# Optimization experiments

Hardware: AMD Instinct MI355X
Metric: run time of the kernel (lower is better)

## Reference

```python
import jax, jax.numpy as jnp
import numpy as np

B, NQ, NKV = 2, 1024, 4096
DQ = 1024          # query_dim == context_dim
H, DH = 16, 64     # heads, dim_head
INNER = H * DH     # 1024
SCALE = DH ** -0.5


def setup_inputs() -> dict:
    key = jax.random.key(0)
    ks = jax.random.split(key, 6)
    s = 1.0 / np.sqrt(DQ)
    return {
        "x": jax.random.normal(ks[0], (B, NQ, DQ), dtype=jnp.float32),
        "context": jax.random.normal(ks[1], (B, NKV, DQ), dtype=jnp.float32),
        "Wq": jax.random.normal(ks[2], (DQ, INNER), dtype=jnp.float32) * s,
        "Wkv": jax.random.normal(ks[3], (DQ, 2 * INNER), dtype=jnp.float32) * s,
        "Wout": jax.random.normal(ks[4], (INNER, DQ), dtype=jnp.float32) * (1.0 / np.sqrt(INNER)),
        "b_out": jax.random.normal(ks[5], (DQ,), dtype=jnp.float32) * 0.01,
    }


def _split_heads(t):
    # b n (h d) -> b h n d
    b, n, _ = t.shape
    return t.reshape(b, n, H, DH).transpose(0, 2, 1, 3)


def reference(x, context, Wq, Wkv, Wout, b_out):
    q = x @ Wq                       # [B, NQ, INNER]
    kv = context @ Wkv               # [B, NKV, 2*INNER]
    k, v = jnp.split(kv, 2, axis=-1)
    q, k, v = map(_split_heads, (q, k, v))          # [B, H, n, DH]
    sim = jnp.einsum("bhid,bhjd->bhij", q, k) * SCALE  # [B, H, NQ, NKV]
    attn = jax.nn.softmax(sim, axis=-1)
    out = jnp.einsum("bhij,bhjd->bhid", attn, v)       # [B, H, NQ, DH]
    out = out.transpose(0, 2, 1, 3).reshape(B, NQ, INNER)  # (b h) n d -> b n (h d)
    return out @ Wout + b_out
```

## Files before the change

kernel.cpp:

```cpp
#include <hip/hip_runtime.h>
#include <stdint.h>

#define B_    2
#define NQ_   1024
#define NKV_  4096
#define DQ_   1024
#define H_    16
#define DH_   64
#define INNER_ 1024

typedef unsigned short u16;
typedef uint32_t u32;
typedef __bf16 bf16x8 __attribute__((ext_vector_type(8)));
typedef float  f32x4  __attribute__((ext_vector_type(4)));

__device__ __forceinline__ u16 f2bf(float x) {
  union { float f; uint32_t u; } v; v.f = x;
  uint32_t r = v.u + 0x7FFFu + ((v.u >> 16) & 1u);
  return (u16)(r >> 16);
}
__device__ __forceinline__ u32 pack2(float a, float b) {
  return (u32)f2bf(a) | ((u32)f2bf(b) << 16);
}
__device__ __forceinline__ u32 pack2rn(float a, float b) {
  union { float f; u32 u; } x, y; x.f = a; y.f = b;
  return __builtin_amdgcn_perm(y.u + 0x8000u, x.u + 0x8000u, 0x07060302u);
}
__device__ __forceinline__ float bf2f(u16 s) {
  union { float f; uint32_t u; } v; v.u = ((uint32_t)s) << 16; return v.f;
}

__device__ __forceinline__ void gload16(const void* g, void* l) {
  __builtin_amdgcn_global_load_lds((const __attribute__((address_space(1))) void*)g,
                                   (__attribute__((address_space(3))) void*)l,
                                   16, 0, 0);
}

__global__ __launch_bounds__(256) void prep(const float* __restrict__ x,
                                            const float* __restrict__ ctx,
                                            const float* __restrict__ Wq,
                                            const float* __restrict__ Wkv,
                                            const float* __restrict__ Wout,
                                            u16* __restrict__ xb,
                                            u16* __restrict__ ctxb,
                                            u16* __restrict__ WqT,
                                            u16* __restrict__ WkvT,
                                            u16* __restrict__ WoutT) {
  int bid = blockIdx.x;
  if (bid < 640) {
    const float* src; u16* dst; int fbase;
    if (bid < 128) { src = x;   dst = xb;   fbase = bid * 4096; }
    else           { src = ctx; dst = ctxb; fbase = (bid - 128) * 4096; }
#pragma unroll
    for (int u = 0; u < 16; ++u) {
      int i = (fbase + u * 256 + threadIdx.x) * 4;
      float4 v = *(const float4*)(src + i);
      uint2 o; o.x = pack2(v.x, v.y); o.y = pack2(v.z, v.w);
      *(uint2*)(dst + i) = o;
    }
    return;
  }
  __shared__ float tile[64][65];
  const float* W; u16* Wt; int K, N, local, ntm;
  int b2 = bid - 640;
  if (b2 < 256)      { W = Wq;   Wt = WqT;   K = 1024; N = 1024; local = b2;       ntm = 15; }
  else if (b2 < 768) { W = Wkv;  Wt = WkvT;  K = 1024; N = 2048; local = b2 - 256; ntm = 31; }
  else               { W = Wout; Wt = WoutT; K = 1024; N = 1024; local = b2 - 768; ntm = 15; }
  int n0 = (local & ntm) * 64;
  int k0 = (local > ntm ? local >> (ntm == 15 ? 4 : 5) : 0) * 64;
  k0 = (ntm == 15) ? (local >> 4) * 64 : (local >> 5) * 64;
  int tx = threadIdx.x & 63, ty = threadIdx.x >> 6;
  for (int i = ty; i < 64; i += 4)
    tile[i][tx] = W[(size_t)(k0 + i) * N + n0 + tx];
  __syncthreads();
  int tx2 = threadIdx.x & 31, ty2 = threadIdx.x >> 5;
  for (int j = ty2; j < 64; j += 8)
    *(u32*)&Wt[(size_t)(n0 + j) * K + k0 + tx2 * 2] =
        pack2(tile[tx2 * 2][j], tile[tx2 * 2 + 1][j]);
}

__global__ __launch_bounds__(512, 2) void kv_gemm(const u16* __restrict__ ctxb,
                                                  const u16* __restrict__ WkvT,
                                                  u16* __restrict__ kb,
                                                  u16* __restrict__ vTb) {
  __shared__ __align__(16) u16 As[2][256 * 64];
  __shared__ __align__(16) u16 Bs[2][256 * 64];
  const int tid = threadIdx.x;
  const int lane = tid & 63;
  const int w = tid >> 6;
  const int wr = w >> 2, wc = w & 3;
  const int l15 = lane & 15, quad = lane >> 4;
  const int K = 1024;

  int bid = blockIdx.x;
  int wgid = (bid & 7) * 32 + (bid >> 3);
  const int tm = wgid >> 3, tn = wgid & 7;
  const int m0 = tm * 256, n0 = tn * 256;
  const u16* Ag = ctxb + (size_t)m0 * K;
  const u16* Bg = WkvT + (size_t)n0 * K;

  size_t offA[2][2], offB[2][2];
#pragma unroll
  for (int ah = 0; ah < 2; ++ah)
#pragma unroll
    for (int p = 0; p < 2; ++p) {
      int c = p * 512 + (w << 6) + lane;
      int s = ah * 128 + (c >> 3);
      int col = ((c & 7) ^ (s & 7)) << 3;
      int rA = ((s >> 6) & 1) * 128 + ((s >> 7) & 1) * 64 + (s & 63);
      int rB = ((s >> 5) & 3) * 64 + ((s >> 7) & 1) * 32 + (s & 31);
      offA[ah][p] = (size_t)rA * 1024 + col;
      offB[ah][p] = (size_t)rB * 1024 + col;
    }

#define STAGE_A(bufi, ah, kk) do { \
    gload16(Ag + offA[ah][0] + (kk), &As[bufi][(ah) * 8192 + (w << 9)]); \
    gload16(Ag + offA[ah][1] + (kk), &As[bufi][(ah) * 8192 + 4096 + (w << 9)]); \
  } while (0)
#define STAGE_B(bufi, bh, kk) do { \
    gload16(Bg + offB[bh][0] + (kk), &Bs[bufi][(bh) * 8192 + (w << 9)]); \
    gload16(Bg + offB[bh][1] + (kk), &Bs[bufi][(bh) * 8192 + 4096 + (w << 9)]); \
  } while (0)
#define LDA2(dst, i8, bufi) do { \
    const int _s = ((i8) >> 2) * 128 + wr * 64 + ((i8) & 3) * 16 + l15; \
    const u16* _p = &As[bufi][_s * 64]; const int _x = _s & 7; \
    dst[0] = *(const bf16x8*)&_p[(quad ^ _x) << 3]; \
    dst[1] = *(const bf16x8*)&_p[((quad + 4) ^ _x) << 3]; \
  } while (0)
#define LDB2(dst, j, bufi) do { \
    const int _s = ((j) >> 1) * 128 + wc * 32 + ((j) & 1) * 16 + l15; \
    const u16* _p = &Bs[bufi][_s * 64]; const int _x = _s & 7; \
    dst[0] = *(const bf16x8*)&_p[(quad ^ _x) << 3]; \
    dst[1] = *(const bf16x8*)&_p[((quad + 4) ^ _x) << 3]; \
  } while (0)
#define MF(i0, j0, bb) do { \
    _Pragma("unroll") \
    for (int _i = 0; _i < 4; ++_i) { \
      acc[(i0) + _i][(j0)    ] = __builtin_amdgcn_mfma_f32_16x16x32_bf16(a[_i][0], bb[0][0], acc[(i0) + _i][(j0)    ], 0, 0, 0); \
      acc[(i0) + _i][(j0)    ] = __builtin_amdgcn_mfma_f32_16x16x32_bf16(a[_i][1], bb[0][1], acc[(i0) + _i][(j0)    ], 0, 0, 0); \
      acc[(i0) + _i][(j0) + 1] = __builtin_amdgcn_mfma_f32_16x16x32_bf16(a[_i][0], bb[1][0], acc[(i0) + _i][(j0) + 1], 0, 0, 0); \
      acc[(i0) + _i][(j0) + 1] = __builtin_amdgcn_mfma_f32_16x16x32_bf16(a[_i][1], bb[1][1], acc[(i0) + _i][(j0) + 1], 0, 0, 0); \
    } \
  } while (0)
#define BAR()   __builtin_amdgcn_s_barrier()
#define LGKM0() asm volatile("s_waitcnt lgkmcnt(0)" ::: "memory")

  f32x4 acc[8][4] = {};
  bf16x8 a[4][2], b[2][2], c2[2][2];

  STAGE_A(0, 0, 0);
  STAGE_B(0, 0, 0);
  STAGE_B(0, 1, 0);
  STAGE_A(0, 1, 0);
  STAGE_A(1, 0, 64);
  STAGE_B(1, 0, 64);
  STAGE_B(1, 1, 64);
  asm volatile("s_waitcnt vmcnt(6)" ::: "memory");
  BAR();

#define HALF(bufi, kAb, kNext, STG, WMID, WEND) do { \
    LDB2(b[0], 0, bufi); LDB2(b[1], 1, bufi); \
    LDA2(a[0], 0, bufi); LDA2(a[1], 1, bufi); LDA2(a[2], 2, bufi); LDA2(a[3], 3, bufi); \
    if (kAb >= 0) STAGE_A((bufi) ^ 1, 1, kAb); \
    BAR(); LGKM0(); \
    __builtin_amdgcn_s_setprio(1); MF(0, 0, b); __builtin_amdgcn_s_setprio(0); \
    BAR(); \
    LDB2(c2[0], 2, bufi); LDB2(c2[1], 3, bufi); \
    if (STG) STAGE_A(bufi, 0, kNext); \
    BAR(); LGKM0(); \
    __builtin_amdgcn_s_setprio(1); MF(0, 2, c2); __builtin_amdgcn_s_setprio(0); \
    BAR(); \
    LDA2(a[0], 4, bufi); LDA2(a[1], 5, bufi); LDA2(a[2], 6, bufi); LDA2(a[3], 7, bufi); \
    if (STG) STAGE_B(bufi, 0, kNext); \
    BAR(); LGKM0(); \
    __builtin_amdgcn_s_setprio(1); MF(4, 0, b); __builtin_amdgcn_s_setprio(0); \
    BAR(); \
    if (STG) STAGE_B(bufi, 1, kNext); \
    BAR(); \
    __builtin_amdgcn_s_setprio(1); MF(4, 2, c2); __builtin_amdgcn_s_setprio(0); \
    WMID; \
    BAR(); \
  } while (0)

  for (int i = 0; i < 7; ++i) {
    const int k2 = i * 128;
    HALF(0, k2 + 64, k2 + 128, 1,
         asm volatile("s_waitcnt vmcnt(6)" ::: "memory"), );
    HALF(1, k2 + 128, k2 + 192, 1,
         asm volatile("s_waitcnt vmcnt(6)" ::: "memory"), );
  }
  HALF(0, 960, 0, 0,
       asm volatile("s_waitcnt vmcnt(0)" ::: "memory"), );
  HALF(1, -1, 0, 0, , );

#undef HALF
#undef BAR
#undef LGKM0

  if (tn < 4) {
#pragma unroll
    for (int i8 = 0; i8 < 8; ++i8)
#pragma unroll
      for (int j = 0; j < 4; ++j) {
        int col = n0 + wc * 64 + j * 16 + l15;
#pragma unroll
        for (int r = 0; r < 4; ++r) {
          int row = m0 + wr * 128 + i8 * 16 + quad * 4 + r;
          kb[(size_t)row * 1024 + col] = f2bf(acc[i8][j][r]);
        }
      }
  } else {
    const int bb_ = m0 >> 12;
#pragma unroll
    for (int i8 = 0; i8 < 8; ++i8) {
      int kvr = (m0 & 4095) + wr * 128 + i8 * 16 + quad * 4;
#pragma unroll
      for (int j = 0; j < 4; ++j) {
        int c = (n0 - 1024) + wc * 64 + j * 16 + l15;
        int h = c >> 6, dh = c & 63;
        uint2 st;
        st.x = pack2(acc[i8][j][0], acc[i8][j][1]);
        st.y = pack2(acc[i8][j][2], acc[i8][j][3]);
        *(uint2*)&vTb[((size_t)((bb_ * 16 + h) * 64 + dh)) * NKV_ + kvr] = st;
      }
    }
  }
#undef STAGE_A
#undef STAGE_B
#undef LDA2
#undef LDB2
#undef MF
}

__global__ __launch_bounds__(256) void out_gemm(const u16* __restrict__ A,
                                                const u16* __restrict__ Bt,
                                                float* __restrict__ Cout,
                                                const float* __restrict__ bias) {
  __shared__ __align__(16) u16 As[3][64 * 32];
  __shared__ __align__(16) u16 Bs[3][128 * 32];
  const int tid = threadIdx.x;
  const int lane = tid & 63;
  const int w = tid >> 6;
  const int wr = w >> 1, wc = w & 1;
  const int l15 = lane & 15, quad = lane >> 4;
  const int unit = blockIdx.x;
  const int m0 = (unit >> 3) * 64, n0 = (unit & 7) * 128;
  const int K = 1024, N = 1024;

  const u16* Ab = A + (size_t)m0 * K;
  const u16* Bb = Bt + (size_t)n0 * K;
  f32x4 acc[2][4] = {};

  const int ar = tid >> 2, ac = (tid & 3) << 3;
  const int q1 = w * 64 + lane, q2 = q1 + 256;
  const int br1 = q1 >> 2, bc1 = (q1 & 3) << 3;
  const int br2 = q2 >> 2, bc2 = (q2 & 3) << 3;

#define STG(bi, k0) do { \
    gload16(Ab + (size_t)ar * K + (k0) + ac, &As[bi][w * 512]); \
    gload16(Bb + (size_t)br1 * K + (k0) + bc1, &Bs[bi][w * 512]); \
    gload16(Bb + (size_t)br2 * K + (k0) + bc2, &Bs[bi][2048 + w * 512]); \
  } while (0)

  STG(0, 0);
  STG(1, 32);
  asm volatile("s_waitcnt vmcnt(3)" ::: "memory");
  __builtin_amdgcn_s_barrier();

  for (int it = 0; it < 32; ++it) {
    const int cur = it % 3;
    bf16x8 af[2], bfr[4];
#pragma unroll
    for (int i = 0; i < 2; ++i)
      af[i] = *(const bf16x8*)&As[cur][(wr * 32 + i * 16 + l15) * 32 + quad * 8];
#pragma unroll
    for (int j = 0; j < 4; ++j)
      bfr[j] = *(const bf16x8*)&Bs[cur][(wc * 64 + j * 16 + l15) * 32 + quad * 8];
    if (it + 2 < 32) STG((it + 2) % 3, (it + 2) * 32);
    __builtin_amdgcn_s_barrier();
    asm volatile("s_waitcnt lgkmcnt(0)" ::: "memory");
    __builtin_amdgcn_s_setprio(1);
#pragma unroll
    for (int i = 0; i < 2; ++i)
#pragma unroll
      for (int j = 0; j < 4; ++j)
        acc[i][j] = __builtin_amdgcn_mfma_f32_16x16x32_bf16(af[i], bfr[j], acc[i][j], 0, 0, 0);
    __builtin_amdgcn_s_setprio(0);
    if (it + 2 < 32)      { asm volatile("s_waitcnt vmcnt(3)" ::: "memory"); }
    else if (it + 2 == 32){ asm volatile("s_waitcnt vmcnt(0)" ::: "memory"); }
    __builtin_amdgcn_s_barrier();
  }
#undef STG

#pragma unroll
  for (int i = 0; i < 2; ++i)
#pragma unroll
    for (int j = 0; j < 4; ++j) {
      int col = n0 + wc * 64 + j * 16 + l15;
      float bv = bias[col];
#pragma unroll
      for (int r = 0; r < 4; ++r) {
        int row = m0 + wr * 32 + i * 16 + quad * 4 + r;
        Cout[(size_t)row * N + col] = acc[i][j][r] + bv;
      }
    }
}

__global__ __launch_bounds__(256, 2) void attn_kernel(const u16* __restrict__ xb,
                                                      const u16* __restrict__ WqT,
                                                      const u16* __restrict__ kb,
                                                      const u16* __restrict__ vT,
                                                      u16* __restrict__ attn_out) {
  __shared__ __align__(16) u16 Ks[128 * 64];
  __shared__ __align__(16) u16 Vs[64 * 128];
  __shared__ __align__(16) u32 P32[4 * 4 * 16 * 20];
  __shared__ float Lr[4][4][16];

  const int tid = threadIdx.x;
  const int lane = tid & 63;
  const int w = tid >> 6;
  const int l15 = lane & 15, quad = lane >> 4;
  const int bh = blockIdx.x, b = bh >> 4, h = bh & 15;
  const int q0 = blockIdx.y * 64;

  const float SC = 0.125f * 1.44269504088896340736f;
  union { u16 s[8]; bf16x8 v; } qf[4][2];

  {
    const u16* Axb = xb + (size_t)(b * NQ_ + q0) * 1024;
    const u16* Bwq = WqT + (size_t)(h * 64) * 1024;
    const int c1 = tid, c2 = tid + 256;
    const int r1 = c1 >> 3, g1 = c1 & 7;
    const int r2 = c2 >> 3, g2 = c2 & 7;
    const size_t sO1 = (size_t)r1 * 1024 + (size_t)((g1 ^ (r1 & 7)) << 3);
    const size_t sO2 = (size_t)r2 * 1024 + (size_t)((g2 ^ (r2 & 7)) << 3);
    f32x4 qacc[4] = {};
    const int x7 = l15 & 7;
    for (int k0 = 0; k0 < 1024; k0 += 64) {
      __syncthreads();
      gload16(Axb + sO1 + k0, &Ks[w * 512]);
      gload16(Axb + sO2 + k0, &Ks[2048 + w * 512]);
      gload16(Bwq + sO1 + k0, &Ks[4096 + w * 512]);
      gload16(Bwq + sO2 + k0, &Ks[6144 + w * 512]);
      __syncthreads();
      bf16x8 af[2], bfr[4][2];
#pragma unroll
      for (int kc = 0; kc < 2; ++kc) {
        af[kc] = *(const bf16x8*)&Ks[(w * 16 + l15) * 64 + (((kc * 4 + quad) ^ x7) << 3)];
#pragma unroll
        for (int j = 0; j < 4; ++j)
          bfr[j][kc] = *(const bf16x8*)
            &Ks[4096 + (j * 16 + l15) * 64 + (((kc * 4 + quad) ^ x7) << 3)];
      }
#pragma unroll
      for (int j = 0; j < 4; ++j) {
        qacc[j] = __builtin_amdgcn_mfma_f32_16x16x32_bf16(af[0], bfr[j][0], qacc[j], 0, 0, 0);
        qacc[j] = __builtin_amdgcn_mfma_f32_16x16x32_bf16(af[1], bfr[j][1], qacc[j], 0, 0, 0);
      }
    }
    float* Q64 = (float*)Vs;
#pragma unroll
    for (int j = 0; j < 4; ++j)
#pragma unroll
      for (int r = 0; r < 4; ++r) {
        int row = w * 16 + quad * 4 + r;
        Q64[row * 64 + ((j * 16 + l15) ^ ((row & 7) * 8))] = qacc[j][r];
      }
    __syncthreads();
#pragma unroll
    for (int t = 0; t < 4; ++t)
#pragma unroll
      for (int kc = 0; kc < 2; ++kc) {
        const float* qp = Q64 + (t * 16 + l15) * 64 + (((kc * 4 + quad) ^ x7) * 8);
        f32x4 lo = *(const f32x4*)qp;
        f32x4 hi = *(const f32x4*)(qp + 4);
#pragma unroll
        for (int e = 0; e < 4; ++e) {
          qf[t][kc].s[e]     = f2bf(lo[e] * SC);
          qf[t][kc].s[e + 4] = f2bf(hi[e] * SC);
        }
      }
    __syncthreads();
  }

#define STAGEKV(j0) do { \
    _Pragma("unroll") \
    for (int i_ = 0; i_ < 4; ++i_) { \
      int s_ = i_ * 256 + tid; \
      int kr = s_ >> 3, kg = (s_ ^ kr) & 7; \
      gload16(kb + (size_t)(b * NKV_ + (j0) + kr) * 1024 + h * 64 + kg * 8, \
              &Ks[(i_ * 256 + w * 64) * 8]); \
      int vr = s_ >> 4, vg = (s_ ^ vr) & 15; \
      gload16(vT + (size_t)(bh * 64 + vr) * NKV_ + (j0) + vg * 8, \
              &Vs[(i_ * 256 + w * 64) * 8]); \
    } \
  } while (0)

  f32x4 Oacc[4][4] = {};
  float l_lane[4] = {0.f, 0.f, 0.f, 0.f};

  STAGEKV(0);

  for (int it = 0; it < 32; ++it) {
    __syncthreads();

    bf16x8 kf[2][2];
#pragma unroll
    for (int kvt = 0; kvt < 2; ++kvt)
#pragma unroll
      for (int kc = 0; kc < 2; ++kc)
        kf[kvt][kc] = *(const bf16x8*)
          &Ks[(w * 32 + kvt * 16 + l15) * 64 + (((kc * 4 + quad) ^ l15) & 7) * 8];
    bf16x8 vf[4];
#pragma unroll
    for (int d = 0; d < 4; ++d)
      vf[d] = *(const bf16x8*)
        &Vs[(d * 16 + l15) * 128 + (((w * 4 + quad) ^ l15) & 15) * 8];

    __syncthreads();

    if (it < 31) STAGEKV((it + 1) * 128);

    f32x4 sacc[2][4] = {};
    __builtin_amdgcn_s_setprio(1);
#pragma unroll
    for (int kvt = 0; kvt < 2; ++kvt)
#pragma unroll
      for (int t = 0; t < 4; ++t)
#pragma unroll
        for (int kc = 0; kc < 2; ++kc)
          sacc[kvt][t] = __builtin_amdgcn_mfma_f32_16x16x32_bf16(
              kf[kvt][kc], qf[t][kc].v, sacc[kvt][t], 0, 0, 0);
    __builtin_amdgcn_s_setprio(0);

#pragma unroll
    for (int kvt = 0; kvt < 2; ++kvt)
#pragma unroll
      for (int t = 0; t < 4; ++t) {
        float p0 = __builtin_amdgcn_exp2f(sacc[kvt][t][0]);
        float p1 = __builtin_amdgcn_exp2f(sacc[kvt][t][1]);
        float p2 = __builtin_amdgcn_exp2f(sacc[kvt][t][2]);
        float p3 = __builtin_amdgcn_exp2f(sacc[kvt][t][3]);
        l_lane[t] += (p0 + p1) + (p2 + p3);
        uint2 pk; pk.x = pack2rn(p0, p1); pk.y = pack2rn(p2, p3);
        *(uint2*)&P32[((w * 4 + t) * 16 + l15) * 20 + kvt * 8 + quad * 2] = pk;
      }

    bf16x8 pf[4];
#pragma unroll
    for (int t = 0; t < 4; ++t)
      pf[t] = *(const bf16x8*)&P32[((w * 4 + t) * 16 + l15) * 20 + quad * 4];
    __builtin_amdgcn_s_setprio(1);
#pragma unroll
    for (int d = 0; d < 4; ++d)
#pragma unroll
      for (int t = 0; t < 4; ++t)
        Oacc[d][t] = __builtin_amdgcn_mfma_f32_16x16x32_bf16(vf[d], pf[t], Oacc[d][t],
                                                             0, 0, 0);
    __builtin_amdgcn_s_setprio(0);
  }
#undef STAGEKV

#pragma unroll
  for (int t = 0; t < 4; ++t) {
    l_lane[t] += __shfl_xor(l_lane[t], 16);
    l_lane[t] += __shfl_xor(l_lane[t], 32);
  }
  if (quad == 0) {
#pragma unroll
    for (int t = 0; t < 4; ++t) Lr[w][t][l15] = l_lane[t];
  }
  __syncthreads();
  float inv = 1.0f / (Lr[0][w][l15] + Lr[1][w][l15] + Lr[2][w][l15] + Lr[3][w][l15]);

  float* red = (float*)P32;
  u16* ob = attn_out + (size_t)(b * NQ_ + q0 + w * 16 + l15) * INNER_ + h * 64;
#pragma unroll
  for (int d = 0; d < 4; ++d) {
    __syncthreads();
#pragma unroll
    for (int t = 0; t < 4; ++t)
      *(f32x4*)&red[(w * 4 + t) * 256 + quad * 64 + l15 * 4] = Oacc[d][t];
    __syncthreads();
    f32x4 r = *(const f32x4*)&red[(0 * 4 + w) * 256 + quad * 64 + l15 * 4];
#pragma unroll
    for (int ww = 1; ww < 4; ++ww) {
      f32x4 c = *(const f32x4*)&red[(ww * 4 + w) * 256 + quad * 64 + l15 * 4];
      r[0] += c[0]; r[1] += c[1]; r[2] += c[2]; r[3] += c[3];
    }
    *(u32*)(ob + d * 16 + quad * 4)     = pack2(r[0] * inv, r[1] * inv);
    *(u32*)(ob + d * 16 + quad * 4 + 2) = pack2(r[2] * inv, r[3] * inv);
  }
}

extern "C" void kernel_launch(void* const* d_in, const int* in_sizes, int n_in,
                              void* d_out, int out_size, void* d_ws, size_t ws_size,
                              hipStream_t stream) {
  const float* x    = (const float*)d_in[0];
  const float* ctx  = (const float*)d_in[1];
  const float* Wq   = (const float*)d_in[2];
  const float* Wkv  = (const float*)d_in[3];
  const float* Wout = (const float*)d_in[4];
  const float* bout = (const float*)d_in[5];

  char* ws = (char*)d_ws;
  u16* xb    = (u16*)(ws + (size_t)( 0u << 20));
  u16* ctxb  = (u16*)(ws + (size_t)( 4u << 20));
  u16* WqT   = (u16*)(ws + (size_t)(20u << 20));
  u16* WkvT  = (u16*)(ws + (size_t)(22u << 20));
  u16* WoutT = (u16*)(ws + (size_t)(26u << 20));
  u16* ab    = (u16*)(ws + (size_t)(28u << 20));
  u16* kb    = (u16*)(ws + (size_t)(32u << 20));
  u16* vTb   = (u16*)(ws + (size_t)(48u << 20));

  prep<<<1664, 256, 0, stream>>>(x, ctx, Wq, Wkv, Wout, xb, ctxb, WqT, WkvT, WoutT);
  kv_gemm<<<256, 512, 0, stream>>>(ctxb, WkvT, kb, vTb);
  attn_kernel<<<dim3(32, 16), 256, 0, stream>>>(xb, WqT, kb, vTb, ab);
  out_gemm<<<256, 256, 0, stream>>>(ab, WoutT, (float*)d_out, bout);
}
```

Measured before the change: 209.1 us.

## Double-buffer fused Q projection loads and use hardware bf16 pack conversion

The Q-projection prologue of the attention kernel now double-buffers its global-to-LDS loads across the Ks and Vs buffers, using explicit vmcnt waits and barriers so the next k-slice loads while MFMAs run on the current one. The Q staging scratch moves to P32 because Vs is now used as a load buffer. The probability packing switches from a manual round-and-permute to the v_cvt_pk_bf16_f32 instruction, which saves ALU work in the softmax loop. Hand-written waitcnt and barrier sequencing is fragile and could cause races if the counts are wrong.

```diff
diff --git a/kernel.cpp b/kernel.cpp
--- a/kernel.cpp
+++ b/kernel.cpp
@@ -22,9 +22,10 @@
 __device__ __forceinline__ u32 pack2(float a, float b) {
   return (u32)f2bf(a) | ((u32)f2bf(b) << 16);
 }
-__device__ __forceinline__ u32 pack2rn(float a, float b) {
-  union { float f; u32 u; } x, y; x.f = a; y.f = b;
-  return __builtin_amdgcn_perm(y.u + 0x8000u, x.u + 0x8000u, 0x07060302u);
+__device__ __forceinline__ u32 cvtpk(float lo, float hi) {
+  u32 r;
+  asm("v_cvt_pk_bf16_f32 %0, %1, %2" : "=v"(r) : "v"(lo), "v"(hi));
+  return r;
 }
 __device__ __forceinline__ float bf2f(u16 s) {
   union { float f; uint32_t u; } v; v.u = ((uint32_t)s) << 16; return v.f;
@@ -67,8 +68,7 @@
   else if (b2 < 768) { W = Wkv;  Wt = WkvT;  K = 1024; N = 2048; local = b2 - 256; ntm = 31; }
   else               { W = Wout; Wt = WoutT; K = 1024; N = 1024; local = b2 - 768; ntm = 15; }
   int n0 = (local & ntm) * 64;
-  int k0 = (local > ntm ? local >> (ntm == 15 ? 4 : 5) : 0) * 64;
-  k0 = (ntm == 15) ? (local >> 4) * 64 : (local >> 5) * 64;
+  int k0 = (ntm == 15) ? (local >> 4) * 64 : (local >> 5) * 64;
   int tx = threadIdx.x & 63, ty = threadIdx.x >> 6;
   for (int i = ty; i < 64; i += 4)
     tile[i][tx] = W[(size_t)(k0 + i) * N + n0 + tx];
@@ -336,29 +336,50 @@
     const size_t sO2 = (size_t)r2 * 1024 + (size_t)((g2 ^ (r2 & 7)) << 3);
     f32x4 qacc[4] = {};
     const int x7 = l15 & 7;
-    for (int k0 = 0; k0 < 1024; k0 += 64) {
-      __syncthreads();
-      gload16(Axb + sO1 + k0, &Ks[w * 512]);
-      gload16(Axb + sO2 + k0, &Ks[2048 + w * 512]);
-      gload16(Bwq + sO1 + k0, &Ks[4096 + w * 512]);
-      gload16(Bwq + sO2 + k0, &Ks[6144 + w * 512]);
-      __syncthreads();
-      bf16x8 af[2], bfr[4][2];
-#pragma unroll
-      for (int kc = 0; kc < 2; ++kc) {
-        af[kc] = *(const bf16x8*)&Ks[(w * 16 + l15) * 64 + (((kc * 4 + quad) ^ x7) << 3)];
-#pragma unroll
-        for (int j = 0; j < 4; ++j)
-          bfr[j][kc] = *(const bf16x8*)
-            &Ks[4096 + (j * 16 + l15) * 64 + (((kc * 4 + quad) ^ x7) << 3)];
-      }
-#pragma unroll
-      for (int j = 0; j < 4; ++j) {
-        qacc[j] = __builtin_amdgcn_mfma_f32_16x16x32_bf16(af[0], bfr[j][0], qacc[j], 0, 0, 0);
-        qacc[j] = __builtin_amdgcn_mfma_f32_16x16x32_bf16(af[1], bfr[j][1], qacc[j], 0, 0, 0);
-      }
+
+#define QSTG(dst, kk) do { \
+      gload16(Axb + sO1 + (kk), &dst[w * 512]); \
+      gload16(Axb + sO2 + (kk), &dst[2048 + w * 512]); \
+      gload16(Bwq + sO1 + (kk), &dst[4096 + w * 512]); \
+      gload16(Bwq + sO2 + (kk), &dst[6144 + w * 512]); \
+    } while (0)
+
+#define QSTEP(dst, kk, DOSTG, W4, W0) do { \
+      bf16x8 af_[2], bfr_[4][2]; \
+      _Pragma("unroll") \
+      for (int kc = 0; kc < 2; ++kc) { \
+        af_[kc] = *(const bf16x8*)&dst[(w * 16 + l15) * 64 + (((kc * 4 + quad) ^ x7) << 3)]; \
+        _Pragma("unroll") \
+        for (int j = 0; j < 4; ++j) \
+          bfr_[j][kc] = *(const bf16x8*) \
+            &dst[4096 + (j * 16 + l15) * 64 + (((kc * 4 + quad) ^ x7) << 3)]; \
+      } \
+      asm volatile("s_waitcnt lgkmcnt(0)" ::: "memory"); \
+      __builtin_amdgcn_s_barrier(); \
+      if (DOSTG) QSTG(dst, kk); \
+      _Pragma("unroll") \
+      for (int j = 0; j < 4; ++j) { \
+        qacc[j] = __builtin_amdgcn_mfma_f32_16x16x32_bf16(af_[0], bfr_[j][0], qacc[j], 0, 0, 0); \
+        qacc[j] = __builtin_amdgcn_mfma_f32_16x16x32_bf16(af_[1], bfr_[j][1], qacc[j], 0, 0, 0); \
+      } \
+      if (W4)      { asm volatile("s_waitcnt vmcnt(4)" ::: "memory"); } \
+      else if (W0) { asm volatile("s_waitcnt vmcnt(0)" ::: "memory"); } \
+      __builtin_amdgcn_s_barrier(); \
+    } while (0)
+
+    QSTG(Ks, 0);
+    QSTG(Vs, 64);
+    asm volatile("s_waitcnt vmcnt(4)" ::: "memory");
+    __builtin_amdgcn_s_barrier();
+#pragma unroll
+    for (int i = 0; i < 16; i += 2) {
+      QSTEP(Ks, (i + 2) * 64, (i + 2) < 16, (i + 2) < 16, (i + 2) == 16);
+      QSTEP(Vs, (i + 3) * 64, (i + 3) < 16, (i + 3) < 16, 0);
     }
-    float* Q64 = (float*)Vs;
+#undef QSTG
+#undef QSTEP
+
+    float* Q64 = (float*)P32;
 #pragma unroll
     for (int j = 0; j < 4; ++j)
 #pragma unroll
@@ -442,7 +463,7 @@
         float p2 = __builtin_amdgcn_exp2f(sacc[kvt][t][2]);
         float p3 = __builtin_amdgcn_exp2f(sacc[kvt][t][3]);
         l_lane[t] += (p0 + p1) + (p2 + p3);
-        uint2 pk; pk.x = pack2rn(p0, p1); pk.y = pack2rn(p2, p3);
+        uint2 pk; pk.x = cvtpk(p0, p1); pk.y = cvtpk(p2, p3);
         *(uint2*)&P32[((w * 4 + t) * 16 + l15) * 20 + kvt * 8 + quad * 2] = pk;
       }
 
```

New measurement: 206.5 us. No clear change (-1.3%).
